# Kernel optimization log

Hardware: AMD Instinct MI355X
Metric: run time of the kernel (lower is better)

## Reference

```python
import jax, jax.numpy as jnp
import numpy as np

DIM = 1024
HEADS = 16
HEAD_DIM = DIM // HEADS
SCALE = HEAD_DIM ** -0.5
B, N = 2, 2048


def setup_inputs() -> dict:
    key = jax.random.key(0)
    ks = jax.random.split(key, 12)
    s = DIM ** -0.5
    return {
        "x_real": jax.random.normal(ks[0], (B, N, DIM), jnp.float32),
        "x_imag": jax.random.normal(ks[1], (B, N, DIM), jnp.float32),
        "Wqkv_r": jax.random.normal(ks[2], (3 * DIM, DIM), jnp.float32) * s,
        "bqkv_r": jax.random.normal(ks[3], (3 * DIM,), jnp.float32) * 0.01,
        "Wqkv_i": jax.random.normal(ks[4], (3 * DIM, DIM), jnp.float32) * s,
        "bqkv_i": jax.random.normal(ks[5], (3 * DIM,), jnp.float32) * 0.01,
        "Wout_r": jax.random.normal(ks[6], (DIM, DIM), jnp.float32) * s,
        "bout_r": jax.random.normal(ks[7], (DIM,), jnp.float32) * 0.01,
        "Wout_i": jax.random.normal(ks[8], (DIM, DIM), jnp.float32) * s,
        "bout_i": jax.random.normal(ks[9], (DIM,), jnp.float32) * 0.01,
    }


def _split_heads(qkv):
    # (B, N, 3*D) -> q, k, v each (B, H, N, hd)
    b, n, _ = qkv.shape
    qkv = qkv.reshape(b, n, 3, HEADS, HEAD_DIM).transpose(2, 0, 3, 1, 4)
    return qkv[0], qkv[1], qkv[2]


def reference(x_real, x_imag, Wqkv_r, bqkv_r, Wqkv_i, bqkv_i,
              Wout_r, bout_r, Wout_i, bout_i):
    b, n, d = x_real.shape
    q_r, k_r, v_r = _split_heads(x_real @ Wqkv_r.T + bqkv_r)
    q_i, k_i, v_i = _split_heads(x_imag @ Wqkv_i.T + bqkv_i)

    # complex score: (q_r + i q_i) (k_r - i k_i)^T pattern per source
    attn_real = (jnp.einsum('bhqd,bhkd->bhqk', q_r, k_r)
                 + jnp.einsum('bhqd,bhkd->bhqk', q_i, k_i)) * SCALE
    attn_imag = (jnp.einsum('bhqd,bhkd->bhqk', q_i, k_r)
                 - jnp.einsum('bhqd,bhkd->bhqk', q_r, k_i)) * SCALE
    attn_mag = jnp.sqrt(attn_real ** 2 + attn_imag ** 2)
    w = jax.nn.softmax(attn_mag, axis=-1)

    out_r = jnp.einsum('bhqk,bhkd->bhqd', w, v_r).transpose(0, 2, 1, 3).reshape(b, n, d)
    out_i = jnp.einsum('bhqk,bhkd->bhqd', w, v_i).transpose(0, 2, 1, 3).reshape(b, n, d)
    out_r = out_r @ Wout_r.T + bout_r
    out_i = out_i @ Wout_i.T + bout_i
    return out_r, out_i
```

## Files before the change

### kernel.cpp

```cpp
#include <hip/hip_runtime.h>


#define DIM_   1024
#define HEADS_ 16
#define HD_    64
#define BB_    2
#define NN_    2048
#define MTOT_  (BB_*NN_)
#define SCALE_ 0.125f

typedef __bf16 bf16;
typedef __bf16 bf16x8 __attribute__((ext_vector_type(8)));
typedef short  s16x8  __attribute__((ext_vector_type(8)));
typedef float  fx4    __attribute__((ext_vector_type(4)));

__device__ __forceinline__ bf16x8 neg8(bf16x8 v) {
    s16x8 s;
    __builtin_memcpy(&s, &v, sizeof(s));
    s ^= (short)0x8000;
    bf16x8 r;
    __builtin_memcpy(&r, &s, sizeof(r));
    return r;
}

__device__ __forceinline__ void gl_lds16(const void* g, void* l) {
    __builtin_amdgcn_global_load_lds(
        (const __attribute__((address_space(1))) unsigned int*)g,
        (__attribute__((address_space(3))) unsigned int*)l, 16, 0, 0);
}

__global__ __launch_bounds__(256) void cvt_prepass(
    const float* __restrict__ xr, const float* __restrict__ xi,
    const float* __restrict__ wqr, const float* __restrict__ wqi,
    const float* __restrict__ wor, const float* __restrict__ woi,
    bf16* __restrict__ xbf, bf16* __restrict__ wqkv, bf16* __restrict__ wout)
{
    const int bid = blockIdx.x;
    const float* src; bf16* dst; int rel;
    if      (bid < 2048) { src = xr;  dst = xbf;           rel = bid; }
    else if (bid < 4096) { src = xi;  dst = xbf + 4194304; rel = bid - 2048; }
    else if (bid < 5632) { src = wqr; dst = wqkv;          rel = bid - 4096; }
    else if (bid < 7168) { src = wqi; dst = wqkv + 3145728; rel = bid - 5632; }
    else if (bid < 7680) { src = wor; dst = wout;          rel = bid - 7168; }
    else                 { src = woi; dst = wout + 1048576; rel = bid - 7680; }
    size_t base = (size_t)rel * 2048 + (size_t)threadIdx.x * 8;
    fx4 a = *(const fx4*)(src + base);
    fx4 b = *(const fx4*)(src + base + 4);
    bf16x8 o;
#pragma unroll
    for (int j = 0; j < 4; ++j) { o[j] = (bf16)a[j]; o[j+4] = (bf16)b[j]; }
    *(bf16x8*)(dst + base) = o;
}

#define GEMM_CORE(Aptr, Bptr)                                                  \
    __shared__ __align__(16) bf16 As[128*64];                                  \
    __shared__ __align__(16) bf16 Bs[128*64];                                  \
    const int tid  = threadIdx.x;                                              \
    const int w    = tid >> 6, lane = tid & 63;                                \
    const int quad = lane >> 4, lc = lane & 15;                                \
    const int wm   = (w >> 1) * 64, wn = (w & 1) * 64;                         \
    const int rj   = lane >> 3;                                                \
    const int sc   = (lane & 7) ^ rj;                                          \
    const fx4 fzero = {0.f, 0.f, 0.f, 0.f};                                    \
    fx4 acc[4][4];                                                             \
    _Pragma("unroll")                                                          \
    for (int mi = 0; mi < 4; ++mi)                                             \
        _Pragma("unroll")                                                      \
        for (int ni = 0; ni < 4; ++ni) acc[mi][ni] = fzero;                    \
    for (int k0 = 0; k0 < DIM_; k0 += 64) {                                    \
        _Pragma("unroll")                                                      \
        for (int j = 0; j < 4; ++j) {                                          \
            int grp = j*4 + w;                                                 \
            int gr  = grp*8 + rj;                                              \
            gl_lds16(Aptr + (size_t)(m0+gr)*DIM_ + k0 + sc*8, As + grp*512);   \
            gl_lds16(Bptr + (size_t)(n0+gr)*DIM_ + k0 + sc*8, Bs + grp*512);   \
        }                                                                      \
        __syncthreads();                                                       \
        bf16x8 af[2][4], bfr[2][4];                                            \
        _Pragma("unroll")                                                      \
        for (int ks = 0; ks < 2; ++ks) {                                       \
            _Pragma("unroll")                                                  \
            for (int mi = 0; mi < 4; ++mi)                                     \
                af[ks][mi] = *(bf16x8*)&As[(wm+mi*16+lc)*64 + (((ks*4+quad)^(lc&7))*8)]; \
            _Pragma("unroll")                                                  \
            for (int ni = 0; ni < 4; ++ni)                                     \
                bfr[ks][ni] = *(bf16x8*)&Bs[(wn+ni*16+lc)*64 + (((ks*4+quad)^(lc&7))*8)]; \
        }                                                                      \
        _Pragma("unroll")                                                      \
        for (int ks = 0; ks < 2; ++ks)                                         \
            _Pragma("unroll")                                                  \
            for (int mi = 0; mi < 4; ++mi)                                     \
                _Pragma("unroll")                                              \
                for (int ni = 0; ni < 4; ++ni)                                 \
                    acc[mi][ni] = __builtin_amdgcn_mfma_f32_16x16x32_bf16(     \
                        af[ks][mi], bfr[ks][ni], acc[mi][ni], 0, 0, 0);        \
        __syncthreads();                                                       \
    }

__global__ __launch_bounds__(256) void qkv_gemm_dma(
    const bf16* __restrict__ xbf, const bf16* __restrict__ wqkv,
    const float* __restrict__ br, const float* __restrict__ bi,
    bf16* __restrict__ qbuf, bf16* __restrict__ kbuf, bf16* __restrict__ vbuf)
{
    const int z = blockIdx.z;
    const bf16* __restrict__ Ap = xbf  + (size_t)z * 4194304;
    const bf16* __restrict__ Bp = wqkv + (size_t)z * 3145728;
    const float* __restrict__ bias = z ? bi : br;
    const int n0 = blockIdx.x * 128;
    const int m0 = blockIdx.y * 128;

    GEMM_CORE(Ap, Bp)

#pragma unroll
    for (int mi = 0; mi < 4; ++mi)
#pragma unroll
        for (int ni = 0; ni < 4; ++ni)
#pragma unroll
            for (int r = 0; r < 4; ++r) {
                int gm = m0 + wm + mi*16 + quad*4 + r;
                int gc = n0 + wn + ni*16 + lc;
                float val = acc[mi][ni][r] + bias[gc];
                bf16 bv = (bf16)val;
                int which = gc >> 10, h = (gc >> 6) & 15, hd = gc & 63;
                int b = gm >> 11, n = gm & 2047;
                size_t base = (size_t)((z*BB_ + b)*HEADS_ + h);
                if (which == 0)      qbuf[(base*NN_ + n)*HD_ + hd] = bv;
                else if (which == 1) kbuf[(base*NN_ + n)*HD_ + hd] = bv;
                else                 vbuf[(base*HD_ + hd)*NN_ + n] = bv;
            }
}

__global__ __launch_bounds__(256) void out_gemm_dma(
    const bf16* __restrict__ obuf, const bf16* __restrict__ wout,
    const float* __restrict__ br, const float* __restrict__ bi,
    float* __restrict__ out)
{
    const int z = blockIdx.z;
    const bf16* __restrict__ Ap = obuf + (size_t)z * 4194304;
    const bf16* __restrict__ Bp = wout + (size_t)z * 1048576;
    const float* __restrict__ bias = z ? bi : br;
    float* __restrict__ dst = out + (size_t)z * 4194304;
    const int n0 = blockIdx.x * 128;
    const int m0 = blockIdx.y * 128;

    GEMM_CORE(Ap, Bp)

#pragma unroll
    for (int mi = 0; mi < 4; ++mi)
#pragma unroll
        for (int ni = 0; ni < 4; ++ni)
#pragma unroll
            for (int r = 0; r < 4; ++r) {
                int gm = m0 + wm + mi*16 + quad*4 + r;
                int gc = n0 + wn + ni*16 + lc;
                dst[(size_t)gm*DIM_ + gc] = acc[mi][ni][r] + bias[gc];
            }
}

#define KT 32
#define NSTEP (NN_/KT)

__global__ __launch_bounds__(256, 2) void attn_fwd(
    const bf16* __restrict__ qbuf, const bf16* __restrict__ kbuf,
    const bf16* __restrict__ vbuf, bf16* __restrict__ obuf)
{
    const int bid = blockIdx.x;
    const int xcd = bid & 7;
    const int i   = bid >> 3;
    const int hb  = xcd*4 + (i >> 4);
    const int blk = i & 15;
    const int b = hb >> 4, h = hb & 15;

    const int tid  = threadIdx.x;
    const int w    = tid >> 6, lane = tid & 63;
    const int quad = lane >> 4, lc = lane & 15;
    const int q0   = blk*128 + w*32;

    __shared__ __align__(16) bf16 KV[2*8192];
    __shared__ __align__(16) bf16 Ps[4*2*32*40];
    bf16* psw = Ps + w*(2*32*40);

    const size_t hR = (size_t)(b)*HEADS_ + h;
    const size_t hI = (size_t)(BB_ + b)*HEADS_ + h;
    const bf16* qrg = qbuf + hR*NN_*HD_;
    const bf16* qig = qbuf + hI*NN_*HD_;
    const char* krg = (const char*)(kbuf + hR*NN_*HD_);
    const char* kig = (const char*)(kbuf + hI*NN_*HD_);
    const char* vrg = (const char*)(vbuf + hR*HD_*NN_);
    const char* vig = (const char*)(vbuf + hI*HD_*NN_);

    bf16x8 qr0[2], qr1[2], qi0[2], qi1[2], nqr0[2], nqr1[2];
#pragma unroll
    for (int band = 0; band < 2; ++band) {
        const bf16* pr = qrg + (size_t)(q0 + band*16 + lc)*HD_ + quad*8;
        const bf16* pi = qig + (size_t)(q0 + band*16 + lc)*HD_ + quad*8;
        qr0[band] = *(const bf16x8*)(pr);
        qr1[band] = *(const bf16x8*)(pr + 32);
        qi0[band] = *(const bf16x8*)(pi);
        qi1[band] = *(const bf16x8*)(pi + 32);
        nqr0[band] = neg8(qr0[band]);
        nqr1[band] = neg8(qr1[band]);
    }

    const char* stg_base;
    size_t lane_off, step_mul, j_mul;
    if (w < 2) {
        stg_base = w ? kig : krg;
        lane_off = (size_t)(lane >> 3)*128 + (size_t)((lane & 7) ^ (lane >> 3))*16;
        step_mul = (size_t)KT * 128;
        j_mul    = 1024;
    } else {
        stg_base = (w == 3) ? vig : vrg;
        lane_off = (size_t)(lane >> 2)*4096 + (size_t)((lane & 3) ^ ((lane >> 2) & 3))*16;
        step_mul = (size_t)KT * 2;
        j_mul    = 65536;
    }
    bf16* lds_arr = KV + w*2048;

    const fx4 fzero = {0.f, 0.f, 0.f, 0.f};
    fx4 O[2][2][4];
    float l_[2][4];
#pragma unroll
    for (int band = 0; band < 2; ++band) {
#pragma unroll
        for (int r = 0; r < 4; ++r) l_[band][r] = 0.f;
#pragma unroll
        for (int ri = 0; ri < 2; ++ri)
#pragma unroll
            for (int vb = 0; vb < 4; ++vb) O[band][ri][vb] = fzero;
    }
    bf16x8 pf[2];
    bf16x8 vf[2][4];

    {
        const char* g = stg_base + lane_off;
#pragma unroll
        for (int j = 0; j < 4; ++j)
            gl_lds16(g + j*j_mul, lds_arr + j*512);
    }
    __syncthreads();

    for (int s = 0; s < NSTEP; ++s) {
        const int buf = s & 1;
        bf16* kvb = KV + buf*8192;

        if (s < NSTEP-1) {
            const char* g = stg_base + (size_t)(s+1)*step_mul + lane_off;
            bf16* l = lds_arr + (buf ^ 1)*8192;
#pragma unroll
            for (int j = 0; j < 4; ++j)
                gl_lds16(g + j*j_mul, l + j*512);
        }

        if (s > 0) {
#pragma unroll
            for (int band = 0; band < 2; ++band)
#pragma unroll
                for (int ri = 0; ri < 2; ++ri)
#pragma unroll
                    for (int vb = 0; vb < 4; ++vb)
                        O[band][ri][vb] = __builtin_amdgcn_mfma_f32_16x16x32_bf16(
                            pf[band], vf[ri][vb], O[band][ri][vb], 0, 0, 0);
        }

        bf16x8 kr_[2][2], ki_[2][2];
#pragma unroll
        for (int kb = 0; kb < 2; ++kb)
#pragma unroll
            for (int half = 0; half < 2; ++half) {
                int r = kb*16 + lc;
                int c = (half*4 + quad) ^ (r & 7);
                kr_[kb][half] = *(bf16x8*)&kvb[0*2048 + r*64 + c*8];
                ki_[kb][half] = *(bf16x8*)&kvb[1*2048 + r*64 + c*8];
            }

#pragma unroll
        for (int band = 0; band < 2; ++band)
#pragma unroll
            for (int kb = 0; kb < 2; ++kb) {
                fx4 sr = fzero, si = fzero;
                sr = __builtin_amdgcn_mfma_f32_16x16x32_bf16(qr0[band],  kr_[kb][0], sr, 0,0,0);
                sr = __builtin_amdgcn_mfma_f32_16x16x32_bf16(qr1[band],  kr_[kb][1], sr, 0,0,0);
                sr = __builtin_amdgcn_mfma_f32_16x16x32_bf16(qi0[band],  ki_[kb][0], sr, 0,0,0);
                sr = __builtin_amdgcn_mfma_f32_16x16x32_bf16(qi1[band],  ki_[kb][1], sr, 0,0,0);
                si = __builtin_amdgcn_mfma_f32_16x16x32_bf16(qi0[band],  kr_[kb][0], si, 0,0,0);
                si = __builtin_amdgcn_mfma_f32_16x16x32_bf16(qi1[band],  kr_[kb][1], si, 0,0,0);
                si = __builtin_amdgcn_mfma_f32_16x16x32_bf16(nqr0[band], ki_[kb][0], si, 0,0,0);
                si = __builtin_amdgcn_mfma_f32_16x16x32_bf16(nqr1[band], ki_[kb][1], si, 0,0,0);
#pragma unroll
                for (int r = 0; r < 4; ++r) {
                    float s2 = sr[r]*sr[r] + si[r]*si[r];
                    float mg = __builtin_amdgcn_sqrtf(s2);
                    float pv = __expf(mg * SCALE_);
                    l_[band][r] += pv;
                    psw[buf*1280 + (band*16 + quad*4 + r)*40 + kb*16 + lc] = (bf16)pv;
                }
            }

#pragma unroll
        for (int band = 0; band < 2; ++band)
            pf[band] = *(bf16x8*)&psw[buf*1280 + (band*16 + lc)*40 + quad*8];
#pragma unroll
        for (int ri = 0; ri < 2; ++ri)
#pragma unroll
            for (int vb = 0; vb < 4; ++vb) {
                int r = vb*16 + lc;
                int c = quad ^ (r & 3);
                vf[ri][vb] = *(bf16x8*)&kvb[(2+ri)*2048 + r*32 + c*8];
            }

        __syncthreads();
    }

#pragma unroll
    for (int band = 0; band < 2; ++band)
#pragma unroll
        for (int ri = 0; ri < 2; ++ri)
#pragma unroll
            for (int vb = 0; vb < 4; ++vb)
                O[band][ri][vb] = __builtin_amdgcn_mfma_f32_16x16x32_bf16(
                    pf[band], vf[ri][vb], O[band][ri][vb], 0, 0, 0);

#pragma unroll
    for (int off = 1; off < 16; off <<= 1)
#pragma unroll
        for (int band = 0; band < 2; ++band)
#pragma unroll
            for (int r = 0; r < 4; ++r)
                l_[band][r] += __shfl_xor(l_[band][r], off);
    float inv[2][4];
#pragma unroll
    for (int band = 0; band < 2; ++band)
#pragma unroll
        for (int r = 0; r < 4; ++r) inv[band][r] = 1.f / l_[band][r];

    bf16* obr = obuf + ((size_t)(b)*NN_)*DIM_;
    bf16* obi = obuf + ((size_t)(BB_ + b)*NN_)*DIM_;
#pragma unroll
    for (int band = 0; band < 2; ++band)
#pragma unroll
        for (int vb = 0; vb < 4; ++vb)
#pragma unroll
            for (int r = 0; r < 4; ++r) {
                int gn = q0 + band*16 + quad*4 + r;
                int gc = h*HD_ + vb*16 + lc;
                obr[(size_t)gn*DIM_ + gc] = (bf16)(O[band][0][vb][r] * inv[band][r]);
                obi[(size_t)gn*DIM_ + gc] = (bf16)(O[band][1][vb][r] * inv[band][r]);
            }
}

__global__ __launch_bounds__(256) void qkv_gemm_legacy(
    const float* __restrict__ xr, const float* __restrict__ xi,
    const float* __restrict__ Wr, const float* __restrict__ Wi,
    const float* __restrict__ br, const float* __restrict__ bi,
    bf16* __restrict__ qbuf, bf16* __restrict__ kbuf, bf16* __restrict__ vbuf)
{
    const int z = blockIdx.z;
    const float* __restrict__ A    = z ? xi : xr;
    const float* __restrict__ W    = z ? Wi : Wr;
    const float* __restrict__ bias = z ? bi : br;
    const int n0 = blockIdx.x * 128;
    const int m0 = blockIdx.y * 128;

    __shared__ bf16 As[128*40];
    __shared__ bf16 Bs[128*40];

    const int tid  = threadIdx.x;
    const int w    = tid >> 6, lane = tid & 63;
    const int quad = lane >> 4, lc = lane & 15;
    const int wm   = (w >> 1) * 64, wn = (w & 1) * 64;

    const fx4 fzero = {0.f, 0.f, 0.f, 0.f};
    fx4 acc[4][4];
#pragma unroll
    for (int mi = 0; mi < 4; ++mi)
#pragma unroll
        for (int ni = 0; ni < 4; ++ni) acc[mi][ni] = fzero;

    for (int k0 = 0; k0 < DIM_; k0 += 32) {
#pragma unroll
        for (int it = 0; it < 2; ++it) {
            int flat = it*2048 + tid*8;
            int row = flat >> 5, col = flat & 31;
            const float* pa = A + (size_t)(m0+row)*DIM_ + k0 + col;
            const float* pb = W + (size_t)(n0+row)*DIM_ + k0 + col;
            fx4 a0 = *(const fx4*)pa, a1 = *(const fx4*)(pa+4);
            fx4 b0 = *(const fx4*)pb, b1 = *(const fx4*)(pb+4);
            bf16x8 av, bv;
#pragma unroll
            for (int j = 0; j < 4; ++j) {
                av[j] = (bf16)a0[j]; av[j+4] = (bf16)a1[j];
                bv[j] = (bf16)b0[j]; bv[j+4] = (bf16)b1[j];
            }
            *(bf16x8*)&As[row*40 + col] = av;
            *(bf16x8*)&Bs[row*40 + col] = bv;
        }
        __syncthreads();

        bf16x8 af[4], bfr[4];
#pragma unroll
        for (int mi = 0; mi < 4; ++mi) af[mi]  = *(bf16x8*)&As[(wm + mi*16 + lc)*40 + quad*8];
#pragma unroll
        for (int ni = 0; ni < 4; ++ni) bfr[ni] = *(bf16x8*)&Bs[(wn + ni*16 + lc)*40 + quad*8];
#pragma unroll
        for (int mi = 0; mi < 4; ++mi)
#pragma unroll
            for (int ni = 0; ni < 4; ++ni)
                acc[mi][ni] = __builtin_amdgcn_mfma_f32_16x16x32_bf16(af[mi], bfr[ni], acc[mi][ni], 0, 0, 0);
        __syncthreads();
    }

#pragma unroll
    for (int mi = 0; mi < 4; ++mi)
#pragma unroll
        for (int ni = 0; ni < 4; ++ni)
#pragma unroll
            for (int r = 0; r < 4; ++r) {
                int gm = m0 + wm + mi*16 + quad*4 + r;
                int gc = n0 + wn + ni*16 + lc;
                float val = acc[mi][ni][r] + bias[gc];
                bf16 bv = (bf16)val;
                int which = gc >> 10, h = (gc >> 6) & 15, hd = gc & 63;
                int b = gm >> 11, n = gm & 2047;
                size_t base = (size_t)((z*BB_ + b)*HEADS_ + h);
                if (which == 0)      qbuf[(base*NN_ + n)*HD_ + hd] = bv;
                else if (which == 1) kbuf[(base*NN_ + n)*HD_ + hd] = bv;
                else                 vbuf[(base*HD_ + hd)*NN_ + n] = bv;
            }
}

__global__ __launch_bounds__(256) void out_gemm_legacy(
    const bf16* __restrict__ obuf,
    const float* __restrict__ Wr, const float* __restrict__ Wi,
    const float* __restrict__ br, const float* __restrict__ bi,
    float* __restrict__ out)
{
    const int z = blockIdx.z;
    const bf16*  __restrict__ A    = obuf + (size_t)z * MTOT_ * DIM_;
    const float* __restrict__ W    = z ? Wi : Wr;
    const float* __restrict__ bias = z ? bi : br;
    float* __restrict__ dst        = out + (size_t)z * MTOT_ * DIM_;
    const int n0 = blockIdx.x * 128;
    const int m0 = blockIdx.y * 128;

    __shared__ bf16 As[128*40];
    __shared__ bf16 Bs[128*40];

    const int tid  = threadIdx.x;
    const int w    = tid >> 6, lane = tid & 63;
    const int quad = lane >> 4, lc = lane & 15;
    const int wm   = (w >> 1) * 64, wn = (w & 1) * 64;

    const fx4 fzero = {0.f, 0.f, 0.f, 0.f};
    fx4 acc[4][4];
#pragma unroll
    for (int mi = 0; mi < 4; ++mi)
#pragma unroll
        for (int ni = 0; ni < 4; ++ni) acc[mi][ni] = fzero;

    for (int k0 = 0; k0 < DIM_; k0 += 32) {
#pragma unroll
        for (int it = 0; it < 2; ++it) {
            int flat = it*2048 + tid*8;
            int row = flat >> 5, col = flat & 31;
            *(bf16x8*)&As[row*40 + col] = *(const bf16x8*)(A + (size_t)(m0+row)*DIM_ + k0 + col);
            const float* pb = W + (size_t)(n0+row)*DIM_ + k0 + col;
            fx4 b0 = *(const fx4*)pb, b1 = *(const fx4*)(pb+4);
            bf16x8 bv;
#pragma unroll
            for (int j = 0; j < 4; ++j) { bv[j] = (bf16)b0[j]; bv[j+4] = (bf16)b1[j]; }
            *(bf16x8*)&Bs[row*40 + col] = bv;
        }
        __syncthreads();

        bf16x8 af[4], bfr[4];
#pragma unroll
        for (int mi = 0; mi < 4; ++mi) af[mi]  = *(bf16x8*)&As[(wm + mi*16 + lc)*40 + quad*8];
#pragma unroll
        for (int ni = 0; ni < 4; ++ni) bfr[ni] = *(bf16x8*)&Bs[(wn + ni*16 + lc)*40 + quad*8];
#pragma unroll
        for (int mi = 0; mi < 4; ++mi)
#pragma unroll
            for (int ni = 0; ni < 4; ++ni)
                acc[mi][ni] = __builtin_amdgcn_mfma_f32_16x16x32_bf16(af[mi], bfr[ni], acc[mi][ni], 0, 0, 0);
        __syncthreads();
    }

#pragma unroll
    for (int mi = 0; mi < 4; ++mi)
#pragma unroll
        for (int ni = 0; ni < 4; ++ni)
#pragma unroll
            for (int r = 0; r < 4; ++r) {
                int gm = m0 + wm + mi*16 + quad*4 + r;
                int gc = n0 + wn + ni*16 + lc;
                dst[(size_t)gm*DIM_ + gc] = acc[mi][ni][r] + bias[gc];
            }
}

extern "C" void kernel_launch(void* const* d_in, const int* in_sizes, int n_in,
                              void* d_out, int out_size, void* d_ws, size_t ws_size,
                              hipStream_t stream) {
    const float* xr  = (const float*)d_in[0];
    const float* xi  = (const float*)d_in[1];
    const float* Wqr = (const float*)d_in[2];
    const float* bqr = (const float*)d_in[3];
    const float* Wqi = (const float*)d_in[4];
    const float* bqi = (const float*)d_in[5];
    const float* Wor = (const float*)d_in[6];
    const float* bor = (const float*)d_in[7];
    const float* Woi = (const float*)d_in[8];
    const float* boi = (const float*)d_in[9];
    float* out = (float*)d_out;

    bf16* ws = (bf16*)d_ws;
    const size_t NEED = 83886080ull;

    if (ws_size >= NEED) {
        bf16* xbf  = ws;
        bf16* wqkv = ws + 8388608;
        bf16* wout = ws + 14680064;
        bf16* qb   = ws + 16777216;
        bf16* kb   = ws + 25165824;
        bf16* vb   = ws + 33554432;
        bf16* obuf = xbf;

        cvt_prepass<<<dim3(8192), 256, 0, stream>>>(xr, xi, Wqr, Wqi, Wor, Woi,
                                                    xbf, wqkv, wout);
        qkv_gemm_dma<<<dim3(24, 32, 2), 256, 0, stream>>>(xbf, wqkv, bqr, bqi,
                                                          qb, kb, vb);
        attn_fwd<<<dim3(512), 256, 0, stream>>>(qb, kb, vb, obuf);
        out_gemm_dma<<<dim3(8, 32, 2), 256, 0, stream>>>(obuf, wout, bor, boi, out);
    } else {
        const size_t per = (size_t)2 * BB_ * HEADS_ * NN_ * HD_;
        bf16* qb   = ws;
        bf16* kb   = ws + per;
        bf16* vb   = ws + 2*per;
        bf16* obuf = ws + 3*per;
        qkv_gemm_legacy<<<dim3(24, 32, 2), 256, 0, stream>>>(xr, xi, Wqr, Wqi,
                                                             bqr, bqi, qb, kb, vb);
        attn_fwd<<<dim3(512), 256, 0, stream>>>(qb, kb, vb, obuf);
        out_gemm_legacy<<<dim3(8, 32, 2), 256, 0, stream>>>(obuf, Wor, Woi,
                                                            bor, boi, out);
    }
}
```

Before: 351.3 us.

## Halve attention query tile per wave and double grid for occupancy

Each attention block now covers 64 queries instead of 128, with one 16-row band per wave. The launch grid doubles to 1024 blocks and launch bounds request 4 blocks per CU, which cuts register use and lets more waves hide latency. The P staging buffer is no longer double-buffered, the V LDS swizzle is changed to reduce bank conflicts, and exp is computed with exp2 on a prescaled argument. The cost is that K/V tiles are reloaded twice as often per query, so global and LDS traffic per unit of work goes up.

```diff
diff --git a/kernel.cpp b/kernel.cpp
--- a/kernel.cpp
+++ b/kernel.cpp
@@ -160,25 +160,25 @@
 #define KT 32
 #define NSTEP (NN_/KT)
 
-__global__ __launch_bounds__(256, 2) void attn_fwd(
+__global__ __launch_bounds__(256, 4) void attn_fwd(
     const bf16* __restrict__ qbuf, const bf16* __restrict__ kbuf,
     const bf16* __restrict__ vbuf, bf16* __restrict__ obuf)
 {
     const int bid = blockIdx.x;
     const int xcd = bid & 7;
-    const int i   = bid >> 3;
-    const int hb  = xcd*4 + (i >> 4);
-    const int blk = i & 15;
+    const int loc = bid >> 3;
+    const int hb  = xcd*4 + (loc >> 5);
+    const int blk = loc & 31;
     const int b = hb >> 4, h = hb & 15;
 
     const int tid  = threadIdx.x;
     const int w    = tid >> 6, lane = tid & 63;
     const int quad = lane >> 4, lc = lane & 15;
-    const int q0   = blk*128 + w*32;
+    const int q0   = blk*64 + w*16;
 
     __shared__ __align__(16) bf16 KV[2*8192];
-    __shared__ __align__(16) bf16 Ps[4*2*32*40];
-    bf16* psw = Ps + w*(2*32*40);
+    __shared__ __align__(16) bf16 Ps[4*16*40];
+    bf16* psw = Ps + w*(16*40);
 
     const size_t hR = (size_t)(b)*HEADS_ + h;
     const size_t hI = (size_t)(BB_ + b)*HEADS_ + h;
@@ -189,18 +189,13 @@
     const char* vrg = (const char*)(vbuf + hR*HD_*NN_);
     const char* vig = (const char*)(vbuf + hI*HD_*NN_);
 
-    bf16x8 qr0[2], qr1[2], qi0[2], qi1[2], nqr0[2], nqr1[2];
-#pragma unroll
-    for (int band = 0; band < 2; ++band) {
-        const bf16* pr = qrg + (size_t)(q0 + band*16 + lc)*HD_ + quad*8;
-        const bf16* pi = qig + (size_t)(q0 + band*16 + lc)*HD_ + quad*8;
-        qr0[band] = *(const bf16x8*)(pr);
-        qr1[band] = *(const bf16x8*)(pr + 32);
-        qi0[band] = *(const bf16x8*)(pi);
-        qi1[band] = *(const bf16x8*)(pi + 32);
-        nqr0[band] = neg8(qr0[band]);
-        nqr1[band] = neg8(qr1[band]);
-    }
+    const bf16* pr = qrg + (size_t)(q0 + lc)*HD_ + quad*8;
+    const bf16* pi = qig + (size_t)(q0 + lc)*HD_ + quad*8;
+    bf16x8 qr0 = *(const bf16x8*)(pr);
+    bf16x8 qr1 = *(const bf16x8*)(pr + 32);
+    bf16x8 qi0 = *(const bf16x8*)(pi);
+    bf16x8 qi1 = *(const bf16x8*)(pi + 32);
+    bf16x8 nqr0 = neg8(qr0), nqr1 = neg8(qr1);
 
     const char* stg_base;
     size_t lane_off, step_mul, j_mul;
@@ -211,26 +206,25 @@
         j_mul    = 1024;
     } else {
         stg_base = (w == 3) ? vig : vrg;
-        lane_off = (size_t)(lane >> 2)*4096 + (size_t)((lane & 3) ^ ((lane >> 2) & 3))*16;
+        lane_off = (size_t)(lane >> 2)*4096 + (size_t)((lane & 3) ^ ((lane >> 3) & 3))*16;
         step_mul = (size_t)KT * 2;
         j_mul    = 65536;
     }
     bf16* lds_arr = KV + w*2048;
 
     const fx4 fzero = {0.f, 0.f, 0.f, 0.f};
-    fx4 O[2][2][4];
-    float l_[2][4];
-#pragma unroll
-    for (int band = 0; band < 2; ++band) {
-#pragma unroll
-        for (int r = 0; r < 4; ++r) l_[band][r] = 0.f;
-#pragma unroll
-        for (int ri = 0; ri < 2; ++ri)
-#pragma unroll
-            for (int vb = 0; vb < 4; ++vb) O[band][ri][vb] = fzero;
-    }
-    bf16x8 pf[2];
+    fx4 O[2][4];
+    float l_[4];
+#pragma unroll
+    for (int r = 0; r < 4; ++r) l_[r] = 0.f;
+#pragma unroll
+    for (int ri = 0; ri < 2; ++ri)
+#pragma unroll
+        for (int vb = 0; vb < 4; ++vb) O[ri][vb] = fzero;
+    bf16x8 pf;
     bf16x8 vf[2][4];
+
+    const float CEXP = SCALE_ * 1.44269504f;
 
     {
         const char* g = stg_base + lane_off;
@@ -254,58 +248,48 @@
 
         if (s > 0) {
 #pragma unroll
-            for (int band = 0; band < 2; ++band)
-#pragma unroll
-                for (int ri = 0; ri < 2; ++ri)
-#pragma unroll
-                    for (int vb = 0; vb < 4; ++vb)
-                        O[band][ri][vb] = __builtin_amdgcn_mfma_f32_16x16x32_bf16(
-                            pf[band], vf[ri][vb], O[band][ri][vb], 0, 0, 0);
+            for (int ri = 0; ri < 2; ++ri)
+#pragma unroll
+                for (int vb = 0; vb < 4; ++vb)
+                    O[ri][vb] = __builtin_amdgcn_mfma_f32_16x16x32_bf16(
+                        pf, vf[ri][vb], O[ri][vb], 0, 0, 0);
         }
 
-        bf16x8 kr_[2][2], ki_[2][2];
-#pragma unroll
-        for (int kb = 0; kb < 2; ++kb)
-#pragma unroll
-            for (int half = 0; half < 2; ++half) {
-                int r = kb*16 + lc;
-                int c = (half*4 + quad) ^ (r & 7);
-                kr_[kb][half] = *(bf16x8*)&kvb[0*2048 + r*64 + c*8];
-                ki_[kb][half] = *(bf16x8*)&kvb[1*2048 + r*64 + c*8];
-            }
-
-#pragma unroll
-        for (int band = 0; band < 2; ++band)
-#pragma unroll
-            for (int kb = 0; kb < 2; ++kb) {
-                fx4 sr = fzero, si = fzero;
-                sr = __builtin_amdgcn_mfma_f32_16x16x32_bf16(qr0[band],  kr_[kb][0], sr, 0,0,0);
-                sr = __builtin_amdgcn_mfma_f32_16x16x32_bf16(qr1[band],  kr_[kb][1], sr, 0,0,0);
-                sr = __builtin_amdgcn_mfma_f32_16x16x32_bf16(qi0[band],  ki_[kb][0], sr, 0,0,0);
-                sr = __builtin_amdgcn_mfma_f32_16x16x32_bf16(qi1[band],  ki_[kb][1], sr, 0,0,0);
-                si = __builtin_amdgcn_mfma_f32_16x16x32_bf16(qi0[band],  kr_[kb][0], si, 0,0,0);
-                si = __builtin_amdgcn_mfma_f32_16x16x32_bf16(qi1[band],  kr_[kb][1], si, 0,0,0);
-                si = __builtin_amdgcn_mfma_f32_16x16x32_bf16(nqr0[band], ki_[kb][0], si, 0,0,0);
-                si = __builtin_amdgcn_mfma_f32_16x16x32_bf16(nqr1[band], ki_[kb][1], si, 0,0,0);
-#pragma unroll
-                for (int r = 0; r < 4; ++r) {
-                    float s2 = sr[r]*sr[r] + si[r]*si[r];
-                    float mg = __builtin_amdgcn_sqrtf(s2);
-                    float pv = __expf(mg * SCALE_);
-                    l_[band][r] += pv;
-                    psw[buf*1280 + (band*16 + quad*4 + r)*40 + kb*16 + lc] = (bf16)pv;
-                }
-            }
-
-#pragma unroll
-        for (int band = 0; band < 2; ++band)
-            pf[band] = *(bf16x8*)&psw[buf*1280 + (band*16 + lc)*40 + quad*8];
+#pragma unroll
+        for (int kb = 0; kb < 2; ++kb) {
+            int r = kb*16 + lc;
+            int c0 = quad ^ (r & 7);
+            int c1 = (4 + quad) ^ (r & 7);
+            bf16x8 kr0f = *(bf16x8*)&kvb[0*2048 + r*64 + c0*8];
+            bf16x8 kr1f = *(bf16x8*)&kvb[0*2048 + r*64 + c1*8];
+            bf16x8 ki0f = *(bf16x8*)&kvb[1*2048 + r*64 + c0*8];
+            bf16x8 ki1f = *(bf16x8*)&kvb[1*2048 + r*64 + c1*8];
+            fx4 sr = fzero, si = fzero;
+            sr = __builtin_amdgcn_mfma_f32_16x16x32_bf16(qr0,  kr0f, sr, 0,0,0);
+            sr = __builtin_amdgcn_mfma_f32_16x16x32_bf16(qr1,  kr1f, sr, 0,0,0);
+            sr = __builtin_amdgcn_mfma_f32_16x16x32_bf16(qi0,  ki0f, sr, 0,0,0);
+            sr = __builtin_amdgcn_mfma_f32_16x16x32_bf16(qi1,  ki1f, sr, 0,0,0);
+            si = __builtin_amdgcn_mfma_f32_16x16x32_bf16(qi0,  kr0f, si, 0,0,0);
+            si = __builtin_amdgcn_mfma_f32_16x16x32_bf16(qi1,  kr1f, si, 0,0,0);
+            si = __builtin_amdgcn_mfma_f32_16x16x32_bf16(nqr0, ki0f, si, 0,0,0);
+            si = __builtin_amdgcn_mfma_f32_16x16x32_bf16(nqr1, ki1f, si, 0,0,0);
+#pragma unroll
+            for (int r4 = 0; r4 < 4; ++r4) {
+                float s2 = sr[r4]*sr[r4] + si[r4]*si[r4];
+                float mg = __builtin_amdgcn_sqrtf(s2);
+                float pv = __builtin_amdgcn_exp2f(mg * CEXP);
+                l_[r4] += pv;
+                psw[(quad*4 + r4)*40 + kb*16 + lc] = (bf16)pv;
+            }
+        }
+
+        pf = *(bf16x8*)&psw[lc*40 + quad*8];
 #pragma unroll
         for (int ri = 0; ri < 2; ++ri)
 #pragma unroll
             for (int vb = 0; vb < 4; ++vb) {
                 int r = vb*16 + lc;
-                int c = quad ^ (r & 3);
+                int c = quad ^ ((r >> 1) & 3);
                 vf[ri][vb] = *(bf16x8*)&kvb[(2+ri)*2048 + r*32 + c*8];
             }
 
@@ -313,40 +297,32 @@
     }
 
 #pragma unroll
-    for (int band = 0; band < 2; ++band)
-#pragma unroll
-        for (int ri = 0; ri < 2; ++ri)
-#pragma unroll
-            for (int vb = 0; vb < 4; ++vb)
-                O[band][ri][vb] = __builtin_amdgcn_mfma_f32_16x16x32_bf16(
-                    pf[band], vf[ri][vb], O[band][ri][vb], 0, 0, 0);
+    for (int ri = 0; ri < 2; ++ri)
+#pragma unroll
+        for (int vb = 0; vb < 4; ++vb)
+            O[ri][vb] = __builtin_amdgcn_mfma_f32_16x16x32_bf16(
+                pf, vf[ri][vb], O[ri][vb], 0, 0, 0);
 
 #pragma unroll
     for (int off = 1; off < 16; off <<= 1)
 #pragma unroll
-        for (int band = 0; band < 2; ++band)
-#pragma unroll
-            for (int r = 0; r < 4; ++r)
-                l_[band][r] += __shfl_xor(l_[band][r], off);
-    float inv[2][4];
-#pragma unroll
-    for (int band = 0; band < 2; ++band)
-#pragma unroll
-        for (int r = 0; r < 4; ++r) inv[band][r] = 1.f / l_[band][r];
+        for (int r = 0; r < 4; ++r)
+            l_[r] += __shfl_xor(l_[r], off);
+    float inv[4];
+#pragma unroll
+    for (int r = 0; r < 4; ++r) inv[r] = 1.f / l_[r];
 
     bf16* obr = obuf + ((size_t)(b)*NN_)*DIM_;
     bf16* obi = obuf + ((size_t)(BB_ + b)*NN_)*DIM_;
 #pragma unroll
-    for (int band = 0; band < 2; ++band)
-#pragma unroll
-        for (int vb = 0; vb < 4; ++vb)
-#pragma unroll
-            for (int r = 0; r < 4; ++r) {
-                int gn = q0 + band*16 + quad*4 + r;
-                int gc = h*HD_ + vb*16 + lc;
-                obr[(size_t)gn*DIM_ + gc] = (bf16)(O[band][0][vb][r] * inv[band][r]);
-                obi[(size_t)gn*DIM_ + gc] = (bf16)(O[band][1][vb][r] * inv[band][r]);
-            }
+    for (int vb = 0; vb < 4; ++vb)
+#pragma unroll
+        for (int r = 0; r < 4; ++r) {
+            int gn = q0 + quad*4 + r;
+            int gc = h*HD_ + vb*16 + lc;
+            obr[(size_t)gn*DIM_ + gc] = (bf16)(O[0][vb][r] * inv[r]);
+            obi[(size_t)gn*DIM_ + gc] = (bf16)(O[1][vb][r] * inv[r]);
+        }
 }
 
 __global__ __launch_bounds__(256) void qkv_gemm_legacy(
@@ -529,7 +505,7 @@
                                                     xbf, wqkv, wout);
         qkv_gemm_dma<<<dim3(24, 32, 2), 256, 0, stream>>>(xbf, wqkv, bqr, bqi,
                                                           qb, kb, vb);
-        attn_fwd<<<dim3(512), 256, 0, stream>>>(qb, kb, vb, obuf);
+        attn_fwd<<<dim3(1024), 256, 0, stream>>>(qb, kb, vb, obuf);
         out_gemm_dma<<<dim3(8, 32, 2), 256, 0, stream>>>(obuf, wout, bor, boi, out);
     } else {
         const size_t per = (size_t)2 * BB_ * HEADS_ * NN_ * HD_;
@@ -539,7 +515,7 @@
         bf16* obuf = ws + 3*per;
         qkv_gemm_legacy<<<dim3(24, 32, 2), 256, 0, stream>>>(xr, xi, Wqr, Wqi,
                                                              bqr, bqi, qb, kb, vb);
-        attn_fwd<<<dim3(512), 256, 0, stream>>>(qb, kb, vb, obuf);
+        attn_fwd<<<dim3(1024), 256, 0, stream>>>(qb, kb, vb, obuf);
         out_gemm_legacy<<<dim3(8, 32, 2), 256, 0, stream>>>(obuf, Wor, Woi,
                                                             bor, boi, out);
     }
```

Measured after the change: 365.9 us. 4.2% more time.
